# Performance work log

Hardware: AMD Instinct MI355X
Metric: run time of the kernel (lower is better)

## Reference

```python
import jax, jax.numpy as jnp
import numpy as np
import math

INPUT_SIZE = 4096
NUM_NEURONS = 4096
ATTN_SIZE = 64
BATCH = 8192


def setup_inputs() -> dict:
    key = jax.random.key(0)
    ks = jax.random.split(key, 10)
    lim_in = 1.0 / math.sqrt(INPUT_SIZE)
    lim_a = 1.0 / math.sqrt(ATTN_SIZE)
    x = jax.random.normal(ks[0], (BATCH, INPUT_SIZE), dtype=jnp.float32)
    # attention linears (torch default uniform(-1/sqrt(fan_in), ...))
    Wq = jax.random.uniform(ks[1], (ATTN_SIZE, INPUT_SIZE), jnp.float32, -lim_in, lim_in)
    bq = jnp.zeros((ATTN_SIZE,), jnp.float32)
    Wk = jax.random.uniform(ks[2], (ATTN_SIZE, INPUT_SIZE), jnp.float32, -lim_in, lim_in)
    bk = jnp.zeros((ATTN_SIZE,), jnp.float32)
    Wv = jax.random.uniform(ks[3], (ATTN_SIZE, INPUT_SIZE), jnp.float32, -lim_in, lim_in)
    bv = jnp.zeros((ATTN_SIZE,), jnp.float32)
    Wo = jax.random.uniform(ks[4], (INPUT_SIZE, ATTN_SIZE), jnp.float32, -lim_a, lim_a)
    bo = jnp.zeros((INPUT_SIZE,), jnp.float32)
    # stacked single-weight neurons: weight ~ N(0,1)*0.01, bias 0
    Wn = jax.random.normal(ks[5], (NUM_NEURONS, INPUT_SIZE), jnp.float32) * 0.01
    bn = jnp.zeros((NUM_NEURONS,), jnp.float32)
    return {"x": x, "Wq": Wq, "bq": bq, "Wk": Wk, "bk": bk,
            "Wv": Wv, "bv": bv, "Wo": Wo, "bo": bo, "Wn": Wn, "bn": bn}


def reference(x, Wq, bq, Wk, bk, Wv, bv, Wo, bo, Wn, bn):
    scale = math.sqrt(ATTN_SIZE)
    # x is treated as a length-1 "sequence" of the full feature vector: [B, 1, S]
    q = x @ Wq.T + bq            # [B, A]
    k = x @ Wk.T + bk            # [B, A]
    v = x @ Wv.T + bv            # [B, A]
    # attention over a single token: softmax of a single score == 1, kept for fidelity
    scores = jnp.sum(q * k, axis=-1, keepdims=True) / scale      # [B, 1]
    attn_w = jax.nn.softmax(scores[:, :, None], axis=-1)          # [B, 1, 1] -> all ones
    attended = attn_w[:, 0, :] * v                                # [B, A] == v
    attn_out = attended @ Wo.T + bo                               # [B, S]
    h = attn_out + x                                              # residual
    # stacked single-weight neurons == one GEMM
    out = h @ Wn.T + bn                                           # [B, N]
    return jax.nn.relu(out)
```

## Files before the change

### kernel.cpp

```cpp
#include <hip/hip_runtime.h>
#include <stdint.h>


typedef unsigned short u16;
typedef float f32x4 __attribute__((ext_vector_type(4)));
typedef __bf16 bf16x8 __attribute__((ext_vector_type(8)));
typedef u16 u16x8 __attribute__((ext_vector_type(8)));

__device__ __forceinline__ float b2f(u16 u) {
  union { unsigned int i; float f; } x; x.i = ((unsigned int)u) << 16; return x.f;
}
__device__ __forceinline__ u16 f2b(float f) {
  union { float f; unsigned int i; } x; x.f = f;
  unsigned int r = x.i + 0x7FFFu + ((x.i >> 16) & 1u);
  return (u16)(r >> 16);
}

__device__ __forceinline__ void gl_lds16(const u16* g, u16* l) {
#if __has_builtin(__builtin_amdgcn_global_load_lds)
  __builtin_amdgcn_global_load_lds((__attribute__((address_space(1))) void*)g,
                                   (__attribute__((address_space(3))) void*)l, 16, 0, 0);
#else
  int lane = threadIdx.x & 63;
  *(u16x8*)(l + lane * 8) = *(const u16x8*)g;
#endif
}

__device__ __forceinline__ f32x4 mfma16(bf16x8 a, bf16x8 b, f32x4 c) {
  return __builtin_amdgcn_mfma_f32_16x16x32_bf16(a, b, c, 0, 0, 0);
}

#define XCH 4194304L
#define WNCH 2097152L
#define TOTG 6324224L
__global__ __launch_bounds__(256) void k_cvt(
    const float* __restrict__ x, const float* __restrict__ Wn,
    const float* __restrict__ Wv, const float* __restrict__ Wo,
    u16* __restrict__ xb, u16* __restrict__ Wnb, u16* __restrict__ Wvb,
    u16* __restrict__ WoT) {
  __shared__ __align__(16) u16 t[64 * 72];
  if (blockIdx.x < 64) {
    const int b = blockIdx.x;
    const int tid = threadIdx.x;
    {
      int k = tid >> 2, a0 = (tid & 3) * 16;
      const float* src = &Wo[(size_t)(b * 64 + k) * 64 + a0];
#pragma unroll
      for (int q = 0; q < 4; ++q) {
        f32x4 v = *(const f32x4*)&src[q * 4];
#pragma unroll
        for (int e = 0; e < 4; ++e) t[k * 72 + a0 + q * 4 + e] = f2b(v[e]);
      }
    }
    __syncthreads();
    {
      int a = tid >> 2, k0 = (tid & 3) * 16;
      u16x8 o0, o1;
#pragma unroll
      for (int j = 0; j < 8; ++j) o0[j] = t[(k0 + j) * 72 + a];
#pragma unroll
      for (int j = 0; j < 8; ++j) o1[j] = t[(k0 + 8 + j) * 72 + a];
      *(u16x8*)&WoT[(size_t)a * 4096 + b * 64 + k0] = o0;
      *(u16x8*)&WoT[(size_t)a * 4096 + b * 64 + k0 + 8] = o1;
    }
    return;
  }
  long i = (long)(blockIdx.x - 64) * 256 + threadIdx.x;
  const long stride = 2048L * 256;
  for (; i < TOTG; i += stride) {
    const float* src; u16* dst; long off;
    if (i < XCH) { src = x; dst = xb; off = i * 8; }
    else if (i < XCH + WNCH) { src = Wn; dst = Wnb; off = (i - XCH) * 8; }
    else { src = Wv; dst = Wvb; off = (i - XCH - WNCH) * 8; }
    f32x4 a = *(const f32x4*)&src[off];
    f32x4 b = *(const f32x4*)&src[off + 4];
    u16x8 o;
#pragma unroll
    for (int e = 0; e < 4; ++e) { o[e] = f2b(a[e]); o[4 + e] = f2b(b[e]); }
    *(u16x8*)&dst[off] = o;
  }
}

#define PBK 128
__device__ void gemm_n64(const u16* __restrict__ A, const u16* __restrict__ B,
                         u16* __restrict__ C, const float* __restrict__ bias,
                         long m0, u16* lA, u16* lB) {
  const int tid = threadIdx.x;
  const int w = tid >> 6, l = tid & 63;
  f32x4 acc[4];
#pragma unroll
  for (int nt = 0; nt < 4; ++nt) acc[nt] = (f32x4)(0.f);

  for (int k0 = 0; k0 < 4096; k0 += PBK) {
    __syncthreads();
#pragma unroll
    for (int i = 0; i < 4; ++i) {
      int row = w * 16 + i * 4 + (l >> 4);
      int p = (l & 15) ^ (i * 4 + (l >> 4));
      gl_lds16(A + (m0 + row) * (long)4096 + k0 + p * 8, lA + (w * 16 + i * 4) * PBK);
      gl_lds16(B + (long)row * 4096 + k0 + p * 8, lB + (w * 16 + i * 4) * PBK);
    }
    __syncthreads();
#pragma unroll
    for (int kk = 0; kk < 4; ++kk) {
      int slotA = ((kk * 4 + (l >> 4)) ^ (l & 15)) * 8;
      bf16x8 af = *(const bf16x8*)&lA[(w * 16 + (l & 15)) * PBK + slotA];
#pragma unroll
      for (int nt = 0; nt < 4; ++nt) {
        bf16x8 bf = *(const bf16x8*)&lB[(nt * 16 + (l & 15)) * PBK + slotA];
        acc[nt] = mfma16(af, bf, acc[nt]);
      }
    }
  }
#pragma unroll
  for (int nt = 0; nt < 4; ++nt) {
    int col = nt * 16 + (l & 15);
    float bb = bias ? bias[col] : 0.f;
#pragma unroll
    for (int r = 0; r < 4; ++r) {
      long row = m0 + w * 16 + (l >> 4) * 4 + r;
      C[row * 64 + col] = f2b(acc[nt][r] + bb);
    }
  }
}

__global__ __launch_bounds__(256, 2) void k_prep(
    const u16* __restrict__ xb, const u16* __restrict__ Wvb, const float* __restrict__ bv,
    const u16* __restrict__ Wnb, const u16* __restrict__ WoT,
    const float* __restrict__ bo, const float* __restrict__ bn,
    u16* __restrict__ V, u16* __restrict__ Wm, float* __restrict__ biasTot) {
  __shared__ __align__(16) u16 lA[64 * PBK];
  __shared__ __align__(16) u16 lB[64 * PBK];
  const int bid = blockIdx.x;
  if (bid < 128) {
    gemm_n64(xb, Wvb, V, bv, (long)bid * 64, lA, lB);
  } else if (bid < 192) {
    gemm_n64(Wnb, WoT, Wm, nullptr, (long)(bid - 128) * 64, lA, lB);
  } else {
    const int w = threadIdx.x >> 6, l = threadIdx.x & 63;
    const int n = (bid - 192) * 4 + w;
    float s = 0.f;
#pragma unroll
    for (int j = 0; j < 8; ++j) {
      int off = (j * 64 + l) * 8;
      u16x8 a = *(const u16x8*)&Wnb[(size_t)n * 4096 + off];
      f32x4 c0 = *(const f32x4*)&bo[off];
      f32x4 c1 = *(const f32x4*)&bo[off + 4];
#pragma unroll
      for (int e = 0; e < 4; ++e) s += b2f(a[e]) * c0[e] + b2f(a[4 + e]) * c1[e];
    }
#pragma unroll
    for (int o = 32; o > 0; o >>= 1) s += __shfl_xor(s, o, 64);
    if (l == 0) biasTot[n] = s + bn[n];
  }
}

__global__ __launch_bounds__(256, 2) void k_main(
    const u16* __restrict__ X, const u16* __restrict__ Wn,
    const u16* __restrict__ V, const u16* __restrict__ Wm,
    const float* __restrict__ biasTot, float* __restrict__ Out) {
  __shared__ __align__(16) u16 smem[24576];
  const int tid = threadIdx.x;
  const int w = tid >> 6, l = tid & 63;
  const int wm = w >> 1, wn = w & 1;
  const long mBase = (long)(blockIdx.x >> 5) * 256;
  const int  nBase = (int)(blockIdx.x & 31) * 128;

  const int rsub = w * 8 + (l >> 3);
  const int swe  = ((l & 7) ^ (l >> 3)) * 8;
  const int ldsS = w * 512;

  const int frow = l & 15, fsl = l >> 4, fx = l & 7;
  const int sl0 = (fsl ^ fx) * 8;
  const int sl1 = ((4 + fsl) ^ fx) * 8;
  const int aB = wm * 8192 + frow * 64;
  const int bB = 16384 + wn * 4096 + frow * 64;

  f32x4 acc[8][4];
#pragma unroll
  for (int mt = 0; mt < 8; ++mt)
#pragma unroll
    for (int nt = 0; nt < 4; ++nt) acc[mt][nt] = (f32x4)(0.f);

  for (int kb = 0; kb < 65; ++kb) {
    const u16 *pA, *pB; long lda, ko;
    if (kb < 64) { pA = X; pB = Wn; lda = 4096; ko = (long)kb * 64; }
    else         { pA = V; pB = Wm; lda = 64;   ko = 0; }
    __syncthreads();
#pragma unroll
    for (int op = 0; op < 8; ++op)
      gl_lds16(pA + (mBase + op * 32 + rsub) * lda + ko + swe,
               smem + op * 2048 + ldsS);
#pragma unroll
    for (int op = 0; op < 4; ++op)
      gl_lds16(pB + ((long)nBase + op * 32 + rsub) * lda + ko + swe,
               smem + 16384 + op * 2048 + ldsS);
    __syncthreads();
#pragma unroll
    for (int kk = 0; kk < 2; ++kk) {
      const int sl = kk ? sl1 : sl0;
      bf16x8 af[8], bf[4];
#pragma unroll
      for (int mt = 0; mt < 8; ++mt)
        af[mt] = *(const bf16x8*)&smem[aB + mt * 1024 + sl];
#pragma unroll
      for (int nt = 0; nt < 4; ++nt)
        bf[nt] = *(const bf16x8*)&smem[bB + nt * 1024 + sl];
      __builtin_amdgcn_s_setprio(1);
#pragma unroll
      for (int mt = 0; mt < 8; ++mt)
#pragma unroll
        for (int nt = 0; nt < 4; ++nt)
          acc[mt][nt] = mfma16(af[mt], bf[nt], acc[mt][nt]);
      __builtin_amdgcn_s_setprio(0);
    }
  }

  __syncthreads();
  float* eb = ((float*)smem) + w * 1024;
  float bt[4];
#pragma unroll
  for (int nt = 0; nt < 4; ++nt) bt[nt] = biasTot[nBase + wn * 64 + nt * 16 + frow];
#pragma unroll
  for (int mt = 0; mt < 8; ++mt) {
#pragma unroll
    for (int nt = 0; nt < 4; ++nt) {
#pragma unroll
      for (int r = 0; r < 4; ++r) {
        float val = acc[mt][nt][r] + bt[nt];
        eb[(fsl * 4 + r) * 64 + nt * 16 + frow] = fmaxf(val, 0.f);
      }
    }
    int rr = l >> 2, c0 = (l & 3) * 16;
    long grow = mBase + wm * 128 + mt * 16 + rr;
    int gcol = nBase + wn * 64 + c0;
    f32x4 o0 = *(const f32x4*)&eb[rr * 64 + c0];
    f32x4 o1 = *(const f32x4*)&eb[rr * 64 + c0 + 4];
    f32x4 o2 = *(const f32x4*)&eb[rr * 64 + c0 + 8];
    f32x4 o3 = *(const f32x4*)&eb[rr * 64 + c0 + 12];
    *(f32x4*)&Out[grow * 4096 + gcol] = o0;
    *(f32x4*)&Out[grow * 4096 + gcol + 4] = o1;
    *(f32x4*)&Out[grow * 4096 + gcol + 8] = o2;
    *(f32x4*)&Out[grow * 4096 + gcol + 12] = o3;
  }
}

extern "C" void kernel_launch(void* const* d_in, const int* in_sizes, int n_in,
                              void* d_out, int out_size, void* d_ws, size_t ws_size,
                              hipStream_t stream) {
  const float* x  = (const float*)d_in[0];
  const float* Wv = (const float*)d_in[5];
  const float* bv = (const float*)d_in[6];
  const float* Wo = (const float*)d_in[7];
  const float* bo = (const float*)d_in[8];
  const float* Wn = (const float*)d_in[9];
  const float* bn = (const float*)d_in[10];
  float* out = (float*)d_out;

  char* ws = (char*)d_ws;
  u16* xb  = (u16*)ws;
  u16* Wnb = (u16*)(ws + (64L << 20));
  u16* Wvb = (u16*)(ws + (96L << 20));
  u16* WoT = (u16*)(ws + (96L << 20) + (512 << 10));
  u16* V   = (u16*)(ws + (97L << 20));
  u16* Wm  = (u16*)(ws + (98L << 20));
  float* biasTot = (float*)(ws + (98L << 20) + (512 << 10));

  k_cvt<<<dim3(2112), dim3(256), 0, stream>>>(x, Wn, Wv, Wo, xb, Wnb, Wvb, WoT);
  k_prep<<<dim3(1216), dim3(256), 0, stream>>>(xb, Wvb, bv, Wnb, WoT, bo, bn, V, Wm, biasTot);
  k_main<<<dim3(1024), dim3(256), 0, stream>>>(xb, Wnb, V, Wm, biasTot, out);
}
```

Measured before the change: 589.2 us.

## Double-buffer LDS tiles with K=32 stages to overlap loads with MFMA

The main GEMM loop now uses two LDS buffers holding 32-wide K slices instead of a single 64-wide buffer. The next slice is prefetched asynchronously while MFMAs run on the current one, leaving one barrier per iteration instead of two. The swizzle pattern is reworked for the 32-element row layout. In exchange there are twice as many iterations, and an extra barrier is added inside the epilogue loop over output tiles.

```diff
diff --git a/kernel.cpp b/kernel.cpp
--- a/kernel.cpp
+++ b/kernel.cpp
@@ -166,15 +166,14 @@
   const long mBase = (long)(blockIdx.x >> 5) * 256;
   const int  nBase = (int)(blockIdx.x & 31) * 128;
 
-  const int rsub = w * 8 + (l >> 3);
-  const int swe  = ((l & 7) ^ (l >> 3)) * 8;
+  const int rowS = w * 16 + (l >> 2);
+  const int gsl  = ((l & 3) ^ ((l >> 3) & 3)) * 8;
   const int ldsS = w * 512;
 
-  const int frow = l & 15, fsl = l >> 4, fx = l & 7;
-  const int sl0 = (fsl ^ fx) * 8;
-  const int sl1 = ((4 + fsl) ^ fx) * 8;
-  const int aB = wm * 8192 + frow * 64;
-  const int bB = 16384 + wn * 4096 + frow * 64;
+  const int frow = l & 15;
+  const int slotE = ((l >> 4) ^ ((frow >> 1) & 3)) * 8;
+  const int aOff = wm * 4096 + frow * 32 + slotE;
+  const int bOff = 8192 + wn * 2048 + frow * 32 + slotE;
 
   f32x4 acc[8][4];
 #pragma unroll
@@ -182,45 +181,48 @@
 #pragma unroll
     for (int nt = 0; nt < 4; ++nt) acc[mt][nt] = (f32x4)(0.f);
 
-  for (int kb = 0; kb < 65; ++kb) {
+  auto stage = [&](int tt, int sb) {
     const u16 *pA, *pB; long lda, ko;
-    if (kb < 64) { pA = X; pB = Wn; lda = 4096; ko = (long)kb * 64; }
-    else         { pA = V; pB = Wm; lda = 64;   ko = 0; }
-    __syncthreads();
-#pragma unroll
-    for (int op = 0; op < 8; ++op)
-      gl_lds16(pA + (mBase + op * 32 + rsub) * lda + ko + swe,
-               smem + op * 2048 + ldsS);
+    if (tt < 128) { pA = X; pB = Wn; lda = 4096; ko = (long)tt * 32; }
+    else         { pA = V; pB = Wm; lda = 64;   ko = (long)(tt - 128) * 32; }
 #pragma unroll
     for (int op = 0; op < 4; ++op)
-      gl_lds16(pB + ((long)nBase + op * 32 + rsub) * lda + ko + swe,
-               smem + 16384 + op * 2048 + ldsS);
-    __syncthreads();
-#pragma unroll
-    for (int kk = 0; kk < 2; ++kk) {
-      const int sl = kk ? sl1 : sl0;
-      bf16x8 af[8], bf[4];
-#pragma unroll
-      for (int mt = 0; mt < 8; ++mt)
-        af[mt] = *(const bf16x8*)&smem[aB + mt * 1024 + sl];
+      gl_lds16(pA + (mBase + op * 64 + rowS) * lda + ko + gsl,
+               smem + sb + op * 2048 + ldsS);
+#pragma unroll
+    for (int op = 0; op < 2; ++op)
+      gl_lds16(pB + ((long)nBase + op * 64 + rowS) * lda + ko + gsl,
+               smem + sb + 8192 + op * 2048 + ldsS);
+  };
+
+  stage(0, 0);
+  __syncthreads();
+
+  for (int t = 0; t < 130; ++t) {
+    const int cb = (t & 1) * 12288;
+    if (t < 129) stage(t + 1, ((t + 1) & 1) * 12288);
+    bf16x8 af[8], bf[4];
+#pragma unroll
+    for (int mt = 0; mt < 8; ++mt)
+      af[mt] = *(const bf16x8*)&smem[cb + aOff + mt * 512];
+#pragma unroll
+    for (int nt = 0; nt < 4; ++nt)
+      bf[nt] = *(const bf16x8*)&smem[cb + bOff + nt * 512];
+    __builtin_amdgcn_s_setprio(1);
+#pragma unroll
+    for (int mt = 0; mt < 8; ++mt)
 #pragma unroll
       for (int nt = 0; nt < 4; ++nt)
-        bf[nt] = *(const bf16x8*)&smem[bB + nt * 1024 + sl];
-      __builtin_amdgcn_s_setprio(1);
-#pragma unroll
-      for (int mt = 0; mt < 8; ++mt)
-#pragma unroll
-        for (int nt = 0; nt < 4; ++nt)
-          acc[mt][nt] = mfma16(af[mt], bf[nt], acc[mt][nt]);
-      __builtin_amdgcn_s_setprio(0);
-    }
-  }
-
-  __syncthreads();
+        acc[mt][nt] = mfma16(af[mt], bf[nt], acc[mt][nt]);
+    __builtin_amdgcn_s_setprio(0);
+    __syncthreads();
+  }
+
   float* eb = ((float*)smem) + w * 1024;
   float bt[4];
 #pragma unroll
   for (int nt = 0; nt < 4; ++nt) bt[nt] = biasTot[nBase + wn * 64 + nt * 16 + frow];
+  const int fsl = l >> 4;
 #pragma unroll
   for (int mt = 0; mt < 8; ++mt) {
 #pragma unroll
@@ -242,6 +244,7 @@
     *(f32x4*)&Out[grow * 4096 + gcol + 4] = o1;
     *(f32x4*)&Out[grow * 4096 + gcol + 8] = o2;
     *(f32x4*)&Out[grow * 4096 + gcol + 12] = o3;
+    __syncthreads();
   }
 }
 
```

Result: slower. 626.5 us (+6.3%).
